# Performance work log

Hardware: AMD Instinct MI355X
Metric: run time of the kernel (lower is better)

The kernel has to match this reference:

```python
import jax, jax.numpy as jnp
import numpy as np

NUM_HEADS = 12
QK_SCALE = 1.0
EPS = 1e-12  # torch.nn.functional.normalize default eps


def _l2norm(t):
    # matches torch F.normalize: x / max(||x||_2, eps) along last axis
    n = jnp.sqrt(jnp.sum(t * t, axis=-1, keepdims=True))
    return t / jnp.maximum(n, EPS)


def setup_inputs() -> dict:
    key = jax.random.key(0)
    k1, k2 = jax.random.split(key)
    B, N, dim = 8, 4096, 768
    x = jax.random.normal(k1, (B, N, 3 * dim), dtype=jnp.float32)
    temperature = jnp.ones((NUM_HEADS, 1, 1), dtype=jnp.float32)
    proj_w = jax.random.normal(k2, (dim, dim), dtype=jnp.float32) * (1.0 / np.sqrt(dim))
    proj_b = jnp.zeros((dim,), dtype=jnp.float32)
    return {"x": x, "temperature": temperature, "proj_w": proj_w, "proj_b": proj_b}


def reference(x, temperature, proj_w, proj_b):
    B, N, C3 = x.shape
    C = C3 // 3
    H = NUM_HEADS
    d = C // H
    # (B, N, 3, H, d) -> (3, B, H, N, d)
    qkv = x.reshape(B, N, 3, H, d).transpose(2, 0, 3, 1, 4)
    q, k, v = qkv[0], qkv[1], qkv[2]
    q = jnp.swapaxes(q, -2, -1) * QK_SCALE   # [B, H, d, N]
    v = jnp.swapaxes(v, -2, -1)              # [B, H, d, N]
    q = _l2norm(q)                           # normalize over tokens N
    k = _l2norm(k)                           # normalize over head dim d (k is [B,H,N,d])
    # cross-covariance attention over channels: [B, H, d, d]
    attn = jnp.einsum('bhdn,bhne->bhde', q, k) * temperature
    attn = jax.nn.softmax(attn, axis=-1)
    out = jnp.einsum('bhde,bhen->bhdn', attn, v)  # [B, H, d, N]
    out = out.transpose(0, 3, 1, 2).reshape(B, N, C)  # [B, N, C]
    out = out @ proj_w.T + proj_b
    return out
```

## Files before the change

kernel.cpp:

```cpp
#include <hip/hip_runtime.h>
#include <hip/hip_bf16.h>

#define BB 8
#define NN 4096
#define HH 12
#define CC 768
#define C3 2304

typedef float  f32x4  __attribute__((ext_vector_type(4)));
typedef __bf16 bf16x8 __attribute__((ext_vector_type(8)));
typedef __bf16 bf16x4 __attribute__((ext_vector_type(4)));

__device__ __forceinline__ void gload16(const void* g, void* l) {
  __builtin_amdgcn_global_load_lds((const __attribute__((address_space(1))) void*)g,
                                   (__attribute__((address_space(3))) void*)l, 16, 0, 0);
}

__global__ __launch_bounds__(256) void k0_vcvt(const float* __restrict__ x,
                                               __bf16* __restrict__ vb) {
  const int idx = blockIdx.x * 256 + threadIdx.x;
  const int bn = idx / 192;
  const int c4 = (idx - bn * 192) * 4;
  const float4 v = *(const float4*)(x + (size_t)bn * C3 + 1536 + c4);
  bf16x4 r;
  r[0] = (__bf16)v.x; r[1] = (__bf16)v.y; r[2] = (__bf16)v.z; r[3] = (__bf16)v.w;
  *(bf16x4*)(vb + (size_t)bn * CC + c4) = r;
}

__global__ __launch_bounds__(256) void k1_logits(const float* __restrict__ x,
                                                 float* __restrict__ Spart,
                                                 float* __restrict__ Qpart) {
  const int slice = blockIdx.x;
  const int h = blockIdx.y, b = blockIdx.z;
  const int tid = threadIdx.x;
  __shared__ __bf16 qT[64][40];
  __shared__ __bf16 kT[64][40];
  __shared__ float  qws[4][64];

  const int t   = tid >> 3;
  const int sub = tid & 7;
  const int w   = tid >> 6, lane = tid & 63;
  const int fr  = lane & 15, fk = lane >> 4;

  const float* qbase = x + (size_t)(b * NN + slice * 512) * C3 + h * 64 + sub * 8;

  float qss8[8];
#pragma unroll
  for (int j = 0; j < 8; ++j) qss8[j] = 0.f;
  f32x4 acc[4];
#pragma unroll
  for (int tn = 0; tn < 4; ++tn) acc[tn] = (f32x4){0.f, 0.f, 0.f, 0.f};

  for (int step = 0; step < 16; ++step) {
    const float* qp = qbase + (size_t)(step * 32 + t) * C3;
    const float4 q0 = *(const float4*)(qp);
    const float4 q1 = *(const float4*)(qp + 4);
    const float4 k0 = *(const float4*)(qp + 768);
    const float4 k1 = *(const float4*)(qp + 772);
    float ss = k0.x * k0.x + k0.y * k0.y + k0.z * k0.z + k0.w * k0.w +
               k1.x * k1.x + k1.y * k1.y + k1.z * k1.z + k1.w * k1.w;
    ss += __shfl_xor(ss, 1);
    ss += __shfl_xor(ss, 2);
    ss += __shfl_xor(ss, 4);
    const float inv = 1.0f / fmaxf(sqrtf(ss), 1e-12f);
    __syncthreads();
    const int c0 = sub * 8;
    qT[c0 + 0][t] = (__bf16)q0.x; qT[c0 + 1][t] = (__bf16)q0.y;
    qT[c0 + 2][t] = (__bf16)q0.z; qT[c0 + 3][t] = (__bf16)q0.w;
    qT[c0 + 4][t] = (__bf16)q1.x; qT[c0 + 5][t] = (__bf16)q1.y;
    qT[c0 + 6][t] = (__bf16)q1.z; qT[c0 + 7][t] = (__bf16)q1.w;
    kT[c0 + 0][t] = (__bf16)(k0.x * inv); kT[c0 + 1][t] = (__bf16)(k0.y * inv);
    kT[c0 + 2][t] = (__bf16)(k0.z * inv); kT[c0 + 3][t] = (__bf16)(k0.w * inv);
    kT[c0 + 4][t] = (__bf16)(k1.x * inv); kT[c0 + 5][t] = (__bf16)(k1.y * inv);
    kT[c0 + 6][t] = (__bf16)(k1.z * inv); kT[c0 + 7][t] = (__bf16)(k1.w * inv);
    qss8[0] = fmaf(q0.x, q0.x, qss8[0]); qss8[1] = fmaf(q0.y, q0.y, qss8[1]);
    qss8[2] = fmaf(q0.z, q0.z, qss8[2]); qss8[3] = fmaf(q0.w, q0.w, qss8[3]);
    qss8[4] = fmaf(q1.x, q1.x, qss8[4]); qss8[5] = fmaf(q1.y, q1.y, qss8[5]);
    qss8[6] = fmaf(q1.z, q1.z, qss8[6]); qss8[7] = fmaf(q1.w, q1.w, qss8[7]);
    __syncthreads();
    const bf16x8 afr = *(const bf16x8*)&qT[w * 16 + fr][fk * 8];
#pragma unroll
    for (int tn = 0; tn < 4; ++tn) {
      const bf16x8 bfr = *(const bf16x8*)&kT[tn * 16 + fr][fk * 8];
      acc[tn] = __builtin_amdgcn_mfma_f32_16x16x32_bf16(afr, bfr, acc[tn], 0, 0, 0);
    }
  }

  const int bh = b * HH + h;
  float* Sp = Spart + ((size_t)(slice * 96 + bh)) * 4096;
#pragma unroll
  for (int tn = 0; tn < 4; ++tn)
#pragma unroll
    for (int rr = 0; rr < 4; ++rr)
      Sp[(w * 16 + fk * 4 + rr) * 64 + tn * 16 + fr] = acc[tn][rr];

#pragma unroll
  for (int j = 0; j < 8; ++j) {
    float v = qss8[j];
    v += __shfl_xor(v, 8);
    v += __shfl_xor(v, 16);
    v += __shfl_xor(v, 32);
    if (lane < 8) qws[w][lane * 8 + j] = v;
  }
  __syncthreads();
  if (tid < 64) {
    const float qs = qws[0][tid] + qws[1][tid] + qws[2][tid] + qws[3][tid];
    Qpart[((size_t)(slice * 96 + bh)) * 64 + tid] = qs;
  }
}

__global__ __launch_bounds__(64) void k2_softmax(const float* __restrict__ Spart,
                                                 const float* __restrict__ Qpart,
                                                 const float* __restrict__ temp,
                                                 float* __restrict__ attn) {
  const int h = blockIdx.x, b = blockIdx.y;
  const int i = threadIdx.x;
  const int bh = b * HH + h;
  float qs = 0.f;
#pragma unroll
  for (int s = 0; s < 8; ++s) qs += Qpart[((size_t)(s * 96 + bh)) * 64 + i];
  float v[64];
#pragma unroll
  for (int j = 0; j < 64; ++j) v[j] = 0.f;
  for (int s = 0; s < 8; ++s) {
    const float* Sp = Spart + ((size_t)(s * 96 + bh)) * 4096 + i * 64;
#pragma unroll
    for (int j = 0; j < 64; j += 4) {
      const float4 t4 = *(const float4*)(Sp + j);
      v[j] += t4.x; v[j + 1] += t4.y; v[j + 2] += t4.z; v[j + 3] += t4.w;
    }
  }
  const float rqs = 1.0f / fmaxf(sqrtf(qs), 1e-12f);
  const float tp  = temp[h] * rqs;
  float m = -3.4e38f;
#pragma unroll
  for (int j = 0; j < 64; ++j) { v[j] *= tp; m = fmaxf(m, v[j]); }
  float s = 0.f;
#pragma unroll
  for (int j = 0; j < 64; ++j) { v[j] = __expf(v[j] - m); s += v[j]; }
  const float inv = 1.0f / s;
  float* Ap = attn + (size_t)bh * 4096 + i * 64;
#pragma unroll
  for (int j = 0; j < 64; ++j) Ap[j] = v[j] * inv;
}

__global__ __launch_bounds__(256) void k3_w2(const float* __restrict__ attn,
                                             const float* __restrict__ pw,
                                             __bf16* __restrict__ W2) {
  const int ct = blockIdx.x, h = blockIdx.y, b = blockIdx.z;
  const int co0 = ct * 64;
  __shared__ float pT[64][65];
  __shared__ float ab[64][64];
  const int tid = threadIdx.x;
  const int r = tid >> 2, c0 = (tid & 3) * 16;
  {
    const float* pp = pw + (size_t)(co0 + r) * CC + h * 64 + c0;
    const float4 p0 = *(const float4*)(pp + 0);
    const float4 p1 = *(const float4*)(pp + 4);
    const float4 p2 = *(const float4*)(pp + 8);
    const float4 p3 = *(const float4*)(pp + 12);
    const float* ap = attn + (size_t)(b * HH + h) * 4096 + r * 64 + c0;
    const float4 a0 = *(const float4*)(ap + 0);
    const float4 a1 = *(const float4*)(ap + 4);
    const float4 a2 = *(const float4*)(ap + 8);
    const float4 a3 = *(const float4*)(ap + 12);
    pT[c0 +  0][r] = p0.x; pT[c0 +  1][r] = p0.y; pT[c0 +  2][r] = p0.z; pT[c0 +  3][r] = p0.w;
    pT[c0 +  4][r] = p1.x; pT[c0 +  5][r] = p1.y; pT[c0 +  6][r] = p1.z; pT[c0 +  7][r] = p1.w;
    pT[c0 +  8][r] = p2.x; pT[c0 +  9][r] = p2.y; pT[c0 + 10][r] = p2.z; pT[c0 + 11][r] = p2.w;
    pT[c0 + 12][r] = p3.x; pT[c0 + 13][r] = p3.y; pT[c0 + 14][r] = p3.z; pT[c0 + 15][r] = p3.w;
    *(float4*)&ab[r][c0 + 0]  = a0;
    *(float4*)&ab[r][c0 + 4]  = a1;
    *(float4*)&ab[r][c0 + 8]  = a2;
    *(float4*)&ab[r][c0 + 12] = a3;
  }
  __syncthreads();
  const int col = tid & 63, jg = tid >> 6;
  float accJ[16];
#pragma unroll
  for (int c = 0; c < 16; ++c) accJ[c] = 0.f;
#pragma unroll 4
  for (int i = 0; i < 64; ++i) {
    const float p = pT[i][col];
    const float4* a4 = (const float4*)&ab[i][jg * 16];
    const float4 A0 = a4[0], A1 = a4[1], A2 = a4[2], A3 = a4[3];
    accJ[0]  = fmaf(p, A0.x, accJ[0]);  accJ[1]  = fmaf(p, A0.y, accJ[1]);
    accJ[2]  = fmaf(p, A0.z, accJ[2]);  accJ[3]  = fmaf(p, A0.w, accJ[3]);
    accJ[4]  = fmaf(p, A1.x, accJ[4]);  accJ[5]  = fmaf(p, A1.y, accJ[5]);
    accJ[6]  = fmaf(p, A1.z, accJ[6]);  accJ[7]  = fmaf(p, A1.w, accJ[7]);
    accJ[8]  = fmaf(p, A2.x, accJ[8]);  accJ[9]  = fmaf(p, A2.y, accJ[9]);
    accJ[10] = fmaf(p, A2.z, accJ[10]); accJ[11] = fmaf(p, A2.w, accJ[11]);
    accJ[12] = fmaf(p, A3.x, accJ[12]); accJ[13] = fmaf(p, A3.y, accJ[13]);
    accJ[14] = fmaf(p, A3.z, accJ[14]); accJ[15] = fmaf(p, A3.w, accJ[15]);
  }
  bf16x8 u0, u1;
#pragma unroll
  for (int c = 0; c < 8; ++c) { u0[c] = (__bf16)accJ[c]; u1[c] = (__bf16)accJ[8 + c]; }
  __bf16* wp = W2 + ((size_t)b * CC + co0 + col) * CC + h * 64 + jg * 16;
  *(bf16x8*)(wp)     = u0;
  *(bf16x8*)(wp + 8) = u1;
}

__global__ __launch_bounds__(256) void k4_gemm(const __bf16* __restrict__ vb,
                                               const __bf16* __restrict__ W2,
                                               const float* __restrict__ pb,
                                               float* __restrict__ out) {
  int id = blockIdx.x;
  const int bz = id / 192;
  const int rem = id - bz * 192;
  const int mg = rem / 48;
  const int idx = rem - mg * 48;
  const int nt = idx >> 3;
  const int mt = mg * 8 + (idx & 7);
  const int m0 = mt * 128, co0 = nt * 128;

  __shared__ __bf16 At[128][32];
  __shared__ __bf16 Bt[128][32];

  const int tid  = threadIdx.x;
  const int w    = tid >> 6, lane = tid & 63;
  const int wm   = w >> 1,   wn   = w & 1;
  const int fr   = lane & 15;
  const int fk   = lane >> 4;

  f32x4 acc[4][4];
#pragma unroll
  for (int tm = 0; tm < 4; ++tm)
#pragma unroll
    for (int tn = 0; tn < 4; ++tn) acc[tm][tn] = (f32x4){0.f, 0.f, 0.f, 0.f};

  const int srow = lane >> 2;
  const int scol = (lane & 3) * 8;
  const __bf16* Ag = vb + (size_t)(bz * NN + m0 + w * 32 + srow) * CC + scol;
  const __bf16* Bg = W2 + ((size_t)bz * CC + co0 + w * 32 + srow) * CC + scol;
  __bf16* lA0 = &At[w * 32][0];
  __bf16* lA1 = &At[w * 32 + 16][0];
  __bf16* lB0 = &Bt[w * 32][0];
  __bf16* lB1 = &Bt[w * 32 + 16][0];

  for (int kk = 0; kk < 24; ++kk) {
    const int kb = kk * 32;
    __syncthreads();
    gload16(Ag + kb,            lA0);
    gload16(Ag + 16 * CC + kb,  lA1);
    gload16(Bg + kb,            lB0);
    gload16(Bg + 16 * CC + kb,  lB1);
    __syncthreads();
    bf16x8 afr[4], bfr[4];
#pragma unroll
    for (int tm = 0; tm < 4; ++tm)
      afr[tm] = *(const bf16x8*)&At[wm * 64 + tm * 16 + fr][fk * 8];
#pragma unroll
    for (int tn = 0; tn < 4; ++tn)
      bfr[tn] = *(const bf16x8*)&Bt[wn * 64 + tn * 16 + fr][fk * 8];
#pragma unroll
    for (int tm = 0; tm < 4; ++tm)
#pragma unroll
      for (int tn = 0; tn < 4; ++tn)
        acc[tm][tn] = __builtin_amdgcn_mfma_f32_16x16x32_bf16(afr[tm], bfr[tn],
                                                              acc[tm][tn], 0, 0, 0);
  }

#pragma unroll
  for (int tn = 0; tn < 4; ++tn) {
    const int co = co0 + wn * 64 + tn * 16 + fr;
    const float bias = pb[co];
#pragma unroll
    for (int tm = 0; tm < 4; ++tm) {
#pragma unroll
      for (int rr = 0; rr < 4; ++rr) {
        const int row = m0 + wm * 64 + tm * 16 + fk * 4 + rr;
        out[(size_t)(bz * NN + row) * CC + co] = acc[tm][tn][rr] + bias;
      }
    }
  }
}

extern "C" void kernel_launch(void* const* d_in, const int* in_sizes, int n_in,
                              void* d_out, int out_size, void* d_ws, size_t ws_size,
                              hipStream_t stream) {
  const float* x    = (const float*)d_in[0];
  const float* temp = (const float*)d_in[1];
  const float* pw   = (const float*)d_in[2];
  const float* pb   = (const float*)d_in[3];
  float* out = (float*)d_out;
  char* ws = (char*)d_ws;

  float*  Spart = (float*)(ws);
  float*  Qpart = (float*)(ws + 12582912);
  float*  attn  = (float*)(ws + 12779520);
  __bf16* W2    = (__bf16*)(ws + 14352384);
  __bf16* vb    = (__bf16*)(ws + 23789568);

  hipLaunchKernelGGL(k0_vcvt,    dim3(24576),    dim3(256), 0, stream, x, vb);
  hipLaunchKernelGGL(k1_logits,  dim3(8, 12, 8), dim3(256), 0, stream, x, Spart, Qpart);
  hipLaunchKernelGGL(k2_softmax, dim3(12, 8),    dim3(64),  0, stream, Spart, Qpart, temp, attn);
  hipLaunchKernelGGL(k3_w2,      dim3(12, 12, 8), dim3(256), 0, stream, attn, pw, W2);
  hipLaunchKernelGGL(k4_gemm,    dim3(1536),     dim3(256), 0, stream, vb, W2, pb, out);
}
```

Before: 532.6 us.

## Fuse V bf16 conversion into logits kernel and parallelize softmax rows

Removes the separate V-conversion kernel and has the logits kernel also load the V slice of each row it already walks, convert it to bf16 and store it. This drops one launch, and the extra V reads now share row locality with the Q/K loads. The softmax kernel now spreads each row across four threads with shuffle reductions and vectorized stores, replacing one thread per row with 64-element register arrays. The fused kernel carries more load traffic per block, which could lengthen it.

```diff
diff --git a/kernel.cpp b/kernel.cpp
--- a/kernel.cpp
+++ b/kernel.cpp
@@ -16,18 +16,8 @@
                                    (__attribute__((address_space(3))) void*)l, 16, 0, 0);
 }
 
-__global__ __launch_bounds__(256) void k0_vcvt(const float* __restrict__ x,
-                                               __bf16* __restrict__ vb) {
-  const int idx = blockIdx.x * 256 + threadIdx.x;
-  const int bn = idx / 192;
-  const int c4 = (idx - bn * 192) * 4;
-  const float4 v = *(const float4*)(x + (size_t)bn * C3 + 1536 + c4);
-  bf16x4 r;
-  r[0] = (__bf16)v.x; r[1] = (__bf16)v.y; r[2] = (__bf16)v.z; r[3] = (__bf16)v.w;
-  *(bf16x4*)(vb + (size_t)bn * CC + c4) = r;
-}
-
 __global__ __launch_bounds__(256) void k1_logits(const float* __restrict__ x,
+                                                 __bf16* __restrict__ vb,
                                                  float* __restrict__ Spart,
                                                  float* __restrict__ Qpart) {
   const int slice = blockIdx.x;
@@ -43,6 +33,7 @@
   const int fr  = lane & 15, fk = lane >> 4;
 
   const float* qbase = x + (size_t)(b * NN + slice * 512) * C3 + h * 64 + sub * 8;
+  __bf16* vbase = vb + (size_t)(b * NN + slice * 512) * CC + h * 64 + sub * 8;
 
   float qss8[8];
 #pragma unroll
@@ -57,12 +48,18 @@
     const float4 q1 = *(const float4*)(qp + 4);
     const float4 k0 = *(const float4*)(qp + 768);
     const float4 k1 = *(const float4*)(qp + 772);
+    const float4 v0 = *(const float4*)(qp + 1536);
+    const float4 v1 = *(const float4*)(qp + 1540);
     float ss = k0.x * k0.x + k0.y * k0.y + k0.z * k0.z + k0.w * k0.w +
                k1.x * k1.x + k1.y * k1.y + k1.z * k1.z + k1.w * k1.w;
     ss += __shfl_xor(ss, 1);
     ss += __shfl_xor(ss, 2);
     ss += __shfl_xor(ss, 4);
     const float inv = 1.0f / fmaxf(sqrtf(ss), 1e-12f);
+    bf16x8 vv;
+    vv[0] = (__bf16)v0.x; vv[1] = (__bf16)v0.y; vv[2] = (__bf16)v0.z; vv[3] = (__bf16)v0.w;
+    vv[4] = (__bf16)v1.x; vv[5] = (__bf16)v1.y; vv[6] = (__bf16)v1.z; vv[7] = (__bf16)v1.w;
+    *(bf16x8*)(vbase + (size_t)(step * 32 + t) * CC) = vv;
     __syncthreads();
     const int c0 = sub * 8;
     qT[c0 + 0][t] = (__bf16)q0.x; qT[c0 + 1][t] = (__bf16)q0.y;
@@ -109,23 +106,25 @@
   }
 }
 
-__global__ __launch_bounds__(64) void k2_softmax(const float* __restrict__ Spart,
-                                                 const float* __restrict__ Qpart,
-                                                 const float* __restrict__ temp,
-                                                 float* __restrict__ attn) {
+__global__ __launch_bounds__(256) void k2_softmax(const float* __restrict__ Spart,
+                                                  const float* __restrict__ Qpart,
+                                                  const float* __restrict__ temp,
+                                                  float* __restrict__ attn) {
   const int h = blockIdx.x, b = blockIdx.y;
-  const int i = threadIdx.x;
+  const int tid = threadIdx.x;
+  const int i  = tid >> 2;
+  const int qq = tid & 3;
   const int bh = b * HH + h;
   float qs = 0.f;
 #pragma unroll
   for (int s = 0; s < 8; ++s) qs += Qpart[((size_t)(s * 96 + bh)) * 64 + i];
-  float v[64];
-#pragma unroll
-  for (int j = 0; j < 64; ++j) v[j] = 0.f;
+  float v[16];
+#pragma unroll
+  for (int j = 0; j < 16; ++j) v[j] = 0.f;
   for (int s = 0; s < 8; ++s) {
-    const float* Sp = Spart + ((size_t)(s * 96 + bh)) * 4096 + i * 64;
-#pragma unroll
-    for (int j = 0; j < 64; j += 4) {
+    const float* Sp = Spart + ((size_t)(s * 96 + bh)) * 4096 + i * 64 + qq * 16;
+#pragma unroll
+    for (int j = 0; j < 16; j += 4) {
       const float4 t4 = *(const float4*)(Sp + j);
       v[j] += t4.x; v[j + 1] += t4.y; v[j + 2] += t4.z; v[j + 3] += t4.w;
     }
@@ -134,14 +133,22 @@
   const float tp  = temp[h] * rqs;
   float m = -3.4e38f;
 #pragma unroll
-  for (int j = 0; j < 64; ++j) { v[j] *= tp; m = fmaxf(m, v[j]); }
+  for (int j = 0; j < 16; ++j) { v[j] *= tp; m = fmaxf(m, v[j]); }
+  m = fmaxf(m, __shfl_xor(m, 1));
+  m = fmaxf(m, __shfl_xor(m, 2));
   float s = 0.f;
 #pragma unroll
-  for (int j = 0; j < 64; ++j) { v[j] = __expf(v[j] - m); s += v[j]; }
+  for (int j = 0; j < 16; ++j) { v[j] = __expf(v[j] - m); s += v[j]; }
+  s += __shfl_xor(s, 1);
+  s += __shfl_xor(s, 2);
   const float inv = 1.0f / s;
-  float* Ap = attn + (size_t)bh * 4096 + i * 64;
-#pragma unroll
-  for (int j = 0; j < 64; ++j) Ap[j] = v[j] * inv;
+  float* Ap = attn + (size_t)bh * 4096 + i * 64 + qq * 16;
+#pragma unroll
+  for (int j = 0; j < 16; j += 4) {
+    float4 o;
+    o.x = v[j] * inv; o.y = v[j + 1] * inv; o.z = v[j + 2] * inv; o.w = v[j + 3] * inv;
+    *(float4*)(Ap + j) = o;
+  }
 }
 
 __global__ __launch_bounds__(256) void k3_w2(const float* __restrict__ attn,
@@ -291,9 +298,8 @@
   __bf16* W2    = (__bf16*)(ws + 14352384);
   __bf16* vb    = (__bf16*)(ws + 23789568);
 
-  hipLaunchKernelGGL(k0_vcvt,    dim3(24576),    dim3(256), 0, stream, x, vb);
-  hipLaunchKernelGGL(k1_logits,  dim3(8, 12, 8), dim3(256), 0, stream, x, Spart, Qpart);
-  hipLaunchKernelGGL(k2_softmax, dim3(12, 8),    dim3(64),  0, stream, Spart, Qpart, temp, attn);
+  hipLaunchKernelGGL(k1_logits,  dim3(8, 12, 8),  dim3(256), 0, stream, x, vb, Spart, Qpart);
+  hipLaunchKernelGGL(k2_softmax, dim3(12, 8),     dim3(256), 0, stream, Spart, Qpart, temp, attn);
   hipLaunchKernelGGL(k3_w2,      dim3(12, 12, 8), dim3(256), 0, stream, attn, pw, W2);
-  hipLaunchKernelGGL(k4_gemm,    dim3(1536),     dim3(256), 0, stream, vb, W2, pb, out);
-}
+  hipLaunchKernelGGL(k4_gemm,    dim3(1536),      dim3(256), 0, stream, vb, W2, pb, out);
+}
```

Measured after the change: 531.5 us. No clear change (-0.2%).
